# Kernel optimization log

Measured on AMD Instinct MI355X. Metric: run time of the kernel, lower is better.

## Reference

```python
import jax, jax.numpy as jnp
import numpy as np

B, S, D, H, DH = 4, 2048, 512, 8, 64  # batch, seq, input_dim, heads, per-head output_dim


def setup_inputs() -> dict:
    key = jax.random.key(0)
    ks = jax.random.split(key, 10)
    scale = 0.02
    inp = {
        "x": jax.random.normal(ks[0], (B, S, D), dtype=jnp.float32),
        "biological_mask": jnp.ones((B, S), dtype=bool),
        "Wq": jax.random.normal(ks[1], (D, H * DH), dtype=jnp.float32) * scale,
        "bq": jnp.zeros((H * DH,), dtype=jnp.float32),
        "Wk": jax.random.normal(ks[2], (D, H * DH), dtype=jnp.float32) * scale,
        "bk": jnp.zeros((H * DH,), dtype=jnp.float32),
        "Wv": jax.random.normal(ks[3], (D, H * DH), dtype=jnp.float32) * scale,
        "bv": jnp.zeros((H * DH,), dtype=jnp.float32),
        "Wo": jax.random.normal(ks[4], (H * DH, DH), dtype=jnp.float32) * scale,
        "bo": jnp.zeros((DH,), dtype=jnp.float32),
        "prior_weight": jnp.full((1,), 0.1, dtype=jnp.float32),
    }
    return inp


def reference(x, biological_mask, Wq, bq, Wk, bk, Wv, bv, Wo, bo, prior_weight):
    b, s, _ = x.shape
    inv_sqrt_dh = jnp.float32(1.0 / np.sqrt(DH))
    # projections -> [B,H,S,DH]
    q = (x @ Wq + bq).reshape(b, s, H, DH).transpose(0, 2, 1, 3)
    k = (x @ Wk + bk).reshape(b, s, H, DH).transpose(0, 2, 1, 3)
    v = (x @ Wv + bv).reshape(b, s, H, DH).transpose(0, 2, 1, 3)
    # scores [B,H,S,S]
    scores = jnp.einsum("bhqd,bhkd->bhqk", q, k) * inv_sqrt_dh
    # biological prior: identity matrix, broadcast over batch and heads
    prior = jnp.eye(s, dtype=scores.dtype)[None, None, :, :]
    scores = scores + prior_weight[0] * prior
    attn = jax.nn.softmax(scores, axis=-1)  # dropout is identity in eval mode
    attended = jnp.einsum("bhqk,bhkd->bhqd", attn, v)
    attended = attended.transpose(0, 2, 1, 3).reshape(b, s, H * DH)
    return attended @ Wo + bo
```

## Files before the change

kernel.cpp:

```cpp
#include <hip/hip_runtime.h>
#include <hip/hip_bf16.h>

#define B_ 4
#define S_ 2048
#define D_ 512
#define H_ 8
#define DH_ 64
#define HD_ 512
#define M_ 8192
#define QKVN 1536
#define QKN 1024
#define LOG2E 1.4426950408889634f

typedef __attribute__((ext_vector_type(8))) short bf16x8;
typedef __attribute__((ext_vector_type(4))) float f32x4;
typedef unsigned short u16;

__device__ inline u16 f2bf(float f) {
    __hip_bfloat16 h = __float2bfloat16(f);
    return *reinterpret_cast<u16*>(&h);
}

__device__ inline void async_cp16(const void* g, void* l) {
    __builtin_amdgcn_global_load_lds(
        (const __attribute__((address_space(1))) unsigned int*)g,
        (__attribute__((address_space(3))) unsigned int*)l, 16, 0, 0);
}

__global__ __launch_bounds__(256) void prep_all(
    const float* __restrict__ x, const float* __restrict__ Wq,
    const float* __restrict__ Wk, const float* __restrict__ Wv,
    const float* __restrict__ Wo, u16* __restrict__ xb,
    u16* __restrict__ WqkvT, u16* __restrict__ WoT)
{
    const int z = blockIdx.z;
    const int tid = threadIdx.x;

    if (z == 4) {
        const int id = blockIdx.y * 64 + blockIdx.x;
#pragma unroll
        for (int it = 0; it < 4; ++it) {
            int i = it * 131072 + id * 256 + tid;
            float4 a = *reinterpret_cast<const float4*>(&x[(size_t)i * 8]);
            float4 b = *reinterpret_cast<const float4*>(&x[(size_t)i * 8 + 4]);
            bf16x8 o;
            o[0] = f2bf(a.x); o[1] = f2bf(a.y); o[2] = f2bf(a.z); o[3] = f2bf(a.w);
            o[4] = f2bf(b.x); o[5] = f2bf(b.y); o[6] = f2bf(b.z); o[7] = f2bf(b.w);
            *reinterpret_cast<bf16x8*>(&xb[(size_t)i * 8]) = o;
        }
        return;
    }

    const float* src; u16* dst; int R, C;
    if (z < 3) { if (blockIdx.x >= 8) return;
                 src = (z == 0) ? Wq : (z == 1) ? Wk : Wv;
                 dst = WqkvT + (size_t)z * 512 * 512; R = 512; C = 512; }
    else       { if (blockIdx.x) return; src = Wo; dst = WoT; R = 512; C = 64; }

    __shared__ u16 T[64][65];
    const int c0 = blockIdx.x * 64, r0 = blockIdx.y * 64;
#pragma unroll
    for (int i = 0; i < 4; ++i) {
        int idx = i * 256 + tid;
        int r = idx >> 4, q4 = (idx & 15) << 2;
        float4 vv = *reinterpret_cast<const float4*>(&src[(size_t)(r0 + r) * C + c0 + q4]);
        T[r][q4 + 0] = f2bf(vv.x); T[r][q4 + 1] = f2bf(vv.y);
        T[r][q4 + 2] = f2bf(vv.z); T[r][q4 + 3] = f2bf(vv.w);
    }
    __syncthreads();
#pragma unroll
    for (int i = 0; i < 2; ++i) {
        int idx = i * 256 + tid;
        int cc = idx >> 3, jj = idx & 7;
        bf16x8 o;
#pragma unroll
        for (int e = 0; e < 8; ++e) o[e] = (short)T[jj * 8 + e][cc];
        *reinterpret_cast<bf16x8*>(&dst[(size_t)(c0 + cc) * R + r0 + jj * 8]) = o;
    }
}

__global__ __launch_bounds__(256) void gemm_qkv(
    const u16* __restrict__ A, const u16* __restrict__ BT,
    const float* __restrict__ bq, const float* __restrict__ bk,
    const float* __restrict__ bv, u16* __restrict__ qk,
    u16* __restrict__ v3, float qscale)
{
    __shared__ __align__(16) u16 As[128 * 64];
    __shared__ __align__(16) u16 Bs[128 * 64];
    const int tid = threadIdx.x, lane = tid & 63, w = tid >> 6;
    const int l15 = lane & 15, l4 = lane >> 4;

    const int bidf = blockIdx.x;
    const int xcd = bidf & 7, pos = bidf >> 3;
    const int swz = xcd * 96 + pos;
    const int by = swz / 12, bx = swz - by * 12;
    const int tm = by * 128, tn = bx * 128;
    const int wm = (w >> 1) * 64, wn = (w & 1) * 64;

    f32x4 acc[4][4] = {};

    for (int k0 = 0; k0 < 512; k0 += 64) {
#pragma unroll
        for (int i = 0; i < 4; ++i) {
            int call = w * 4 + i;
            int c = call * 64 + lane;
            int r = c >> 3, j = c & 7;
            async_cp16(A + (size_t)(tm + r) * 512 + k0 + ((j ^ (r & 7)) << 3),
                       &As[call * 512]);
            async_cp16(BT + (size_t)(tn + r) * 512 + k0 + ((j ^ (r & 7)) << 3),
                       &Bs[call * 512]);
        }
        __syncthreads();
#pragma unroll
        for (int ks = 0; ks < 2; ++ks) {
            bf16x8 af[4], bf[4];
#pragma unroll
            for (int mf = 0; mf < 4; ++mf) {
                int r = wm + mf * 16 + l15;
                int j = ks * 4 + l4;
                af[mf] = *reinterpret_cast<const bf16x8*>(&As[(r * 8 + (j ^ (r & 7))) * 8]);
            }
#pragma unroll
            for (int nf = 0; nf < 4; ++nf) {
                int r = wn + nf * 16 + l15;
                int j = ks * 4 + l4;
                bf[nf] = *reinterpret_cast<const bf16x8*>(&Bs[(r * 8 + (j ^ (r & 7))) * 8]);
            }
#pragma unroll
            for (int mf = 0; mf < 4; ++mf)
#pragma unroll
                for (int nf = 0; nf < 4; ++nf)
                    acc[mf][nf] = __builtin_amdgcn_mfma_f32_16x16x32_bf16(
                        af[mf], bf[nf], acc[mf][nf], 0, 0, 0);
        }
        __syncthreads();
    }
#pragma unroll
    for (int nf = 0; nf < 4; ++nf) {
        const int col = tn + wn + nf * 16 + l15;
        if (col < QKN) {
            const float bias_v = (col < 512) ? bq[col] : bk[col - 512];
            const float scl = (col < 512) ? qscale : 1.0f;
#pragma unroll
            for (int mf = 0; mf < 4; ++mf)
#pragma unroll
                for (int r = 0; r < 4; ++r) {
                    int row = tm + wm + mf * 16 + l4 * 4 + r;
                    qk[(size_t)row * QKN + col] = f2bf((acc[mf][nf][r] + bias_v) * scl);
                }
        } else {
            const int dcol = col - QKN;
            const float bias_v = bv[dcol];
            const int hh = dcol >> 6, d64 = dcol & 63;
            const int n = d64 >> 4, dd = d64 & 15;
#pragma unroll
            for (int mf = 0; mf < 4; ++mf) {
                int row0 = tm + wm + mf * 16 + l4 * 4;
                int b = row0 >> 11, s = row0 & 2047;
                int t = s >> 6, s6 = s & 63;
                int ks = s6 >> 5, l4i = (s6 >> 3) & 3, kvi = s6 & 7;
                ushort4 pk;
                pk.x = f2bf(acc[mf][nf][0] + bias_v);
                pk.y = f2bf(acc[mf][nf][1] + bias_v);
                pk.z = f2bf(acc[mf][nf][2] + bias_v);
                pk.w = f2bf(acc[mf][nf][3] + bias_v);
                size_t idx = (((((size_t)(b * 8 + hh) * 32 + t) * 4 + n) * 2 + ks) * 4
                              + l4i) * 128 + dd * 8 + kvi;
                *reinterpret_cast<ushort4*>(&v3[idx]) = pk;
            }
        }
    }
}

__global__ __launch_bounds__(256, 4) void flash_mfma(
    const u16* __restrict__ qk, const u16* __restrict__ v3,
    const float* __restrict__ pw_ptr, u16* __restrict__ att)
{
    __shared__ __align__(16) u16 Kb[2][4096];

    const int tid = threadIdx.x, lane = tid & 63, w = tid >> 6;
    const int l15 = lane & 15, l4 = lane >> 4;
    const int bid = blockIdx.x;
    const int x = bid & 7, g = bid >> 3;
    const int bh = x * 4 + (g >> 5), qt = g & 31;
    const int h = bh & 7, b = bh >> 3;
    const float pwl = pw_ptr[0] * LOG2E;

    const u16* qbase = qk + (size_t)b * S_ * QKN + h * 64;
    const u16* kbase = qbase + 512;
    const u16* vbase = v3 + (size_t)bh * 32 * 4 * 2 * 512 + l4 * 128 + l15 * 8;

    const int qrow0 = qt * 64 + w * 16;
    bf16x8 qb[2];
#pragma unroll
    for (int ks2 = 0; ks2 < 2; ++ks2)
        qb[ks2] = *reinterpret_cast<const bf16x8*>(
            &qbase[(size_t)(qrow0 + l15) * QKN + ks2 * 32 + l4 * 8]);

    const bf16x8 ones = {(short)0x3F80, (short)0x3F80, (short)0x3F80, (short)0x3F80,
                         (short)0x3F80, (short)0x3F80, (short)0x3F80, (short)0x3F80};

    f32x4 accv[4] = {};
    f32x4 accl = {};
    const int diag_t = qt;

#define STAGE(buf, jj) do {                                                        \
    _Pragma("unroll")                                                              \
    for (int i_ = 0; i_ < 2; ++i_) {                                               \
        int call_ = w * 2 + i_;                                                    \
        int c_ = call_ * 64 + lane;                                                \
        int rho_ = c_ >> 3, j_ = c_ & 7;                                           \
        int pi_ = (rho_ & 32) | ((rho_ & 12) << 1) | ((rho_ & 16) >> 2)            \
                | (rho_ & 3);                                                      \
        async_cp16(kbase + (size_t)((jj) + pi_) * QKN + ((j_ ^ (rho_ & 7)) << 3),  \
                   &Kb[buf][call_ * 512]);                                         \
    } } while (0)

    STAGE(0, 0);
    __syncthreads();
    int cur = 0;

    for (int t = 0; t < 32; ++t) {
        const int j0 = t << 6;
        const u16* vt = vbase + (size_t)t * 4096;

        bf16x8 vb01[2][2];
#pragma unroll
        for (int n = 0; n < 2; ++n)
#pragma unroll
            for (int ks = 0; ks < 2; ++ks)
                vb01[n][ks] = *reinterpret_cast<const bf16x8*>(
                    vt + (n * 2 + ks) * 512);

        if (t < 31) STAGE(cur ^ 1, j0 + 64);

        f32x4 s[4] = {};
        __builtin_amdgcn_s_setprio(1);
#pragma unroll
        for (int c = 0; c < 4; ++c)
#pragma unroll
            for (int ks2 = 0; ks2 < 2; ++ks2) {
                const int rr = c * 16 + l15;
                const int sl = ks2 * 4 + l4;
                bf16x8 ka = *reinterpret_cast<const bf16x8*>(
                    &Kb[cur][(rr * 8 + (sl ^ (rr & 7))) * 8]);
                s[c] = __builtin_amdgcn_mfma_f32_16x16x32_bf16(ka, qb[ks2], s[c], 0, 0, 0);
            }
        __builtin_amdgcn_s_setprio(0);

        bf16x8 vb23[2][2];
#pragma unroll
        for (int n = 0; n < 2; ++n)
#pragma unroll
            for (int ks = 0; ks < 2; ++ks)
                vb23[n][ks] = *reinterpret_cast<const bf16x8*>(
                    vt + ((n + 2) * 2 + ks) * 512);

        if (t == diag_t) {
#pragma unroll
            for (int c = 0; c < 4; ++c)
#pragma unroll
                for (int r = 0; r < 4; ++r) {
                    int kv = (c >> 1) * 32 + l4 * 8 + (c & 1) * 4 + r;
                    if (j0 + kv == qrow0 + l15) s[c][r] += pwl;
                }
        }

        bf16x8 pa[2];
#pragma unroll
        for (int ks = 0; ks < 2; ++ks)
#pragma unroll
            for (int d2 = 0; d2 < 2; ++d2)
#pragma unroll
                for (int r = 0; r < 4; ++r)
                    pa[ks][d2 * 4 + r] = (short)f2bf(exp2f(s[ks * 2 + d2][r]));

        __builtin_amdgcn_s_setprio(1);
        accl = __builtin_amdgcn_mfma_f32_16x16x32_bf16(pa[0], ones, accl, 0, 0, 0);
        accl = __builtin_amdgcn_mfma_f32_16x16x32_bf16(pa[1], ones, accl, 0, 0, 0);
#pragma unroll
        for (int n = 0; n < 2; ++n)
#pragma unroll
            for (int ks = 0; ks < 2; ++ks)
                accv[n] = __builtin_amdgcn_mfma_f32_16x16x32_bf16(
                    pa[ks], vb01[n][ks], accv[n], 0, 0, 0);
#pragma unroll
        for (int n = 0; n < 2; ++n)
#pragma unroll
            for (int ks = 0; ks < 2; ++ks)
                accv[n + 2] = __builtin_amdgcn_mfma_f32_16x16x32_bf16(
                    pa[ks], vb23[n][ks], accv[n + 2], 0, 0, 0);
        __builtin_amdgcn_s_setprio(0);

        __syncthreads();
        cur ^= 1;
    }
#undef STAGE

#pragma unroll
    for (int r = 0; r < 4; ++r) {
        float inv = 1.0f / accl[r];
        int row = qrow0 + l4 * 4 + r;
#pragma unroll
        for (int nf = 0; nf < 4; ++nf)
            att[(size_t)(b * S_ + row) * HD_ + h * 64 + nf * 16 + l15] =
                f2bf(accv[nf][r] * inv);
    }
}

__global__ __launch_bounds__(64) void out_proj(
    const u16* __restrict__ att, const u16* __restrict__ WoT,
    const float* __restrict__ bo, float* __restrict__ out)
{
    const int lane = threadIdx.x;
    const int l15 = lane & 15, l4 = lane >> 4;
    const int row0 = blockIdx.x * 16;

    f32x4 acc[4] = {};
#pragma unroll 4
    for (int ks = 0; ks < 16; ++ks) {
        bf16x8 a = *reinterpret_cast<const bf16x8*>(
            &att[(size_t)(row0 + l15) * 512 + ks * 32 + l4 * 8]);
#pragma unroll
        for (int nf = 0; nf < 4; ++nf) {
            bf16x8 bb = *reinterpret_cast<const bf16x8*>(
                &WoT[(size_t)(nf * 16 + l15) * 512 + ks * 32 + l4 * 8]);
            acc[nf] = __builtin_amdgcn_mfma_f32_16x16x32_bf16(a, bb, acc[nf], 0, 0, 0);
        }
    }
#pragma unroll
    for (int nf = 0; nf < 4; ++nf) {
        int n = nf * 16 + l15;
        float bias_v = bo[n];
#pragma unroll
        for (int r = 0; r < 4; ++r)
            out[(size_t)(row0 + l4 * 4 + r) * 64 + n] = acc[nf][r] + bias_v;
    }
}

extern "C" void kernel_launch(void* const* d_in, const int* in_sizes, int n_in,
                              void* d_out, int out_size, void* d_ws, size_t ws_size,
                              hipStream_t stream)
{
    const float* x  = (const float*)d_in[0];
    const float* Wq = (const float*)d_in[2];
    const float* bq = (const float*)d_in[3];
    const float* Wk = (const float*)d_in[4];
    const float* bk = (const float*)d_in[5];
    const float* Wv = (const float*)d_in[6];
    const float* bv = (const float*)d_in[7];
    const float* Wo = (const float*)d_in[8];
    const float* bo = (const float*)d_in[9];
    const float* pw = (const float*)d_in[10];

    u16* ws = (u16*)d_ws;
    size_t o = 0;
    u16* xb    = ws + o; o += (size_t)M_ * D_;
    u16* WqkvT = ws + o; o += (size_t)QKVN * D_;
    u16* WoT   = ws + o; o += (size_t)DH_ * HD_;
    u16* qkb   = ws + o; o += (size_t)M_ * QKN;
    u16* v3b   = ws + o; o += (size_t)M_ * HD_;
    u16* att   = ws + o; o += (size_t)M_ * HD_;

    dim3 blk(256);
    prep_all<<<dim3(64, 8, 5), blk, 0, stream>>>(x, Wq, Wk, Wv, Wo, xb, WqkvT, WoT);

    gemm_qkv<<<dim3(768), blk, 0, stream>>>(
        xb, WqkvT, bq, bk, bv, qkb, v3b, 0.125f * LOG2E);

    flash_mfma<<<dim3(1024), blk, 0, stream>>>(qkb, v3b, pw, att);

    out_proj<<<dim3(M_ / 16), dim3(64), 0, stream>>>(att, WoT, bo, (float*)d_out);
}
```

Measured before the change: 99.68 us.

## Stage 128-key K tiles per barrier in flash kernel and split-K out_proj

The flash attention kernel now stages 128 K rows per double-buffer slot and processes two 64-key halves between barriers. This halves the number of __syncthreads and async-copy rounds, at the cost of doubling K shared memory to 32 KB per block, which may limit occupancy. The output projection moves to 256-thread blocks covering 32 rows, with a two-way split over K whose partial sums are reduced through shared memory. This gives fewer, fuller blocks.

Result: no change. 98.87 us (median of 3 runs) (-0.8%).

```diff
diff --git a/kernel.cpp b/kernel.cpp
--- a/kernel.cpp
+++ b/kernel.cpp
@@ -176,7 +176,7 @@
     const u16* __restrict__ qk, const u16* __restrict__ v3,
     const float* __restrict__ pw_ptr, u16* __restrict__ att)
 {
-    __shared__ __align__(16) u16 Kb[2][4096];
+    __shared__ __align__(16) u16 Kb[2][8192];
 
     const int tid = threadIdx.x, lane = tid & 63, w = tid >> 6;
     const int l15 = lane & 15, l4 = lane >> 4;
@@ -202,100 +202,105 @@
 
     f32x4 accv[4] = {};
     f32x4 accl = {};
-    const int diag_t = qt;
-
-#define STAGE(buf, jj) do {                                                        \
+
+#define STAGE2(buf, jj) do {                                                       \
     _Pragma("unroll")                                                              \
-    for (int i_ = 0; i_ < 2; ++i_) {                                               \
-        int call_ = w * 2 + i_;                                                    \
+    for (int i_ = 0; i_ < 4; ++i_) {                                               \
+        int call_ = w * 4 + i_;                                                    \
         int c_ = call_ * 64 + lane;                                                \
         int rho_ = c_ >> 3, j_ = c_ & 7;                                           \
-        int pi_ = (rho_ & 32) | ((rho_ & 12) << 1) | ((rho_ & 16) >> 2)            \
-                | (rho_ & 3);                                                      \
-        async_cp16(kbase + (size_t)((jj) + pi_) * QKN + ((j_ ^ (rho_ & 7)) << 3),  \
+        int r6_ = rho_ & 63;                                                       \
+        int pi_ = (rho_ & 64) | (r6_ & 32) | ((r6_ & 12) << 1)                     \
+                | ((r6_ & 16) >> 2) | (r6_ & 3);                                   \
+        async_cp16(kbase + (size_t)((jj) + pi_) * QKN + ((j_ ^ (r6_ & 7)) << 3),   \
                    &Kb[buf][call_ * 512]);                                         \
     } } while (0)
 
-    STAGE(0, 0);
+    STAGE2(0, 0);
     __syncthreads();
     int cur = 0;
 
-    for (int t = 0; t < 32; ++t) {
-        const int j0 = t << 6;
-        const u16* vt = vbase + (size_t)t * 4096;
-
-        bf16x8 vb01[2][2];
-#pragma unroll
-        for (int n = 0; n < 2; ++n)
+    for (int t = 0; t < 16; ++t) {
+        if (t < 15) STAGE2(cur ^ 1, (t + 1) << 7);
+
+#pragma unroll
+        for (int half = 0; half < 2; ++half) {
+            const int t2 = t * 2 + half;
+            const int j0h = t2 << 6;
+            const u16* vt = vbase + (size_t)t2 * 4096;
+            const u16* kb = &Kb[cur][half * 4096];
+
+            bf16x8 vb01[2][2];
+#pragma unroll
+            for (int n = 0; n < 2; ++n)
+#pragma unroll
+                for (int ks = 0; ks < 2; ++ks)
+                    vb01[n][ks] = *reinterpret_cast<const bf16x8*>(
+                        vt + (n * 2 + ks) * 512);
+
+            f32x4 s[4] = {};
+            __builtin_amdgcn_s_setprio(1);
+#pragma unroll
+            for (int c = 0; c < 4; ++c)
+#pragma unroll
+                for (int ks2 = 0; ks2 < 2; ++ks2) {
+                    const int rr = c * 16 + l15;
+                    const int sl = ks2 * 4 + l4;
+                    bf16x8 ka = *reinterpret_cast<const bf16x8*>(
+                        &kb[(rr * 8 + (sl ^ (rr & 7))) * 8]);
+                    s[c] = __builtin_amdgcn_mfma_f32_16x16x32_bf16(ka, qb[ks2], s[c], 0, 0, 0);
+                }
+            __builtin_amdgcn_s_setprio(0);
+
+            bf16x8 vb23[2][2];
+#pragma unroll
+            for (int n = 0; n < 2; ++n)
+#pragma unroll
+                for (int ks = 0; ks < 2; ++ks)
+                    vb23[n][ks] = *reinterpret_cast<const bf16x8*>(
+                        vt + ((n + 2) * 2 + ks) * 512);
+
+            if (t2 == qt) {
+#pragma unroll
+                for (int c = 0; c < 4; ++c)
+#pragma unroll
+                    for (int r = 0; r < 4; ++r) {
+                        int kv = (c >> 1) * 32 + l4 * 8 + (c & 1) * 4 + r;
+                        if (j0h + kv == qrow0 + l15) s[c][r] += pwl;
+                    }
+            }
+
+            bf16x8 pa[2];
 #pragma unroll
             for (int ks = 0; ks < 2; ++ks)
-                vb01[n][ks] = *reinterpret_cast<const bf16x8*>(
-                    vt + (n * 2 + ks) * 512);
-
-        if (t < 31) STAGE(cur ^ 1, j0 + 64);
-
-        f32x4 s[4] = {};
-        __builtin_amdgcn_s_setprio(1);
-#pragma unroll
-        for (int c = 0; c < 4; ++c)
-#pragma unroll
-            for (int ks2 = 0; ks2 < 2; ++ks2) {
-                const int rr = c * 16 + l15;
-                const int sl = ks2 * 4 + l4;
-                bf16x8 ka = *reinterpret_cast<const bf16x8*>(
-                    &Kb[cur][(rr * 8 + (sl ^ (rr & 7))) * 8]);
-                s[c] = __builtin_amdgcn_mfma_f32_16x16x32_bf16(ka, qb[ks2], s[c], 0, 0, 0);
-            }
-        __builtin_amdgcn_s_setprio(0);
-
-        bf16x8 vb23[2][2];
-#pragma unroll
-        for (int n = 0; n < 2; ++n)
-#pragma unroll
-            for (int ks = 0; ks < 2; ++ks)
-                vb23[n][ks] = *reinterpret_cast<const bf16x8*>(
-                    vt + ((n + 2) * 2 + ks) * 512);
-
-        if (t == diag_t) {
-#pragma unroll
-            for (int c = 0; c < 4; ++c)
-#pragma unroll
-                for (int r = 0; r < 4; ++r) {
-                    int kv = (c >> 1) * 32 + l4 * 8 + (c & 1) * 4 + r;
-                    if (j0 + kv == qrow0 + l15) s[c][r] += pwl;
-                }
-        }
-
-        bf16x8 pa[2];
-#pragma unroll
-        for (int ks = 0; ks < 2; ++ks)
-#pragma unroll
-            for (int d2 = 0; d2 < 2; ++d2)
-#pragma unroll
-                for (int r = 0; r < 4; ++r)
-                    pa[ks][d2 * 4 + r] = (short)f2bf(exp2f(s[ks * 2 + d2][r]));
-
-        __builtin_amdgcn_s_setprio(1);
-        accl = __builtin_amdgcn_mfma_f32_16x16x32_bf16(pa[0], ones, accl, 0, 0, 0);
-        accl = __builtin_amdgcn_mfma_f32_16x16x32_bf16(pa[1], ones, accl, 0, 0, 0);
-#pragma unroll
-        for (int n = 0; n < 2; ++n)
-#pragma unroll
-            for (int ks = 0; ks < 2; ++ks)
-                accv[n] = __builtin_amdgcn_mfma_f32_16x16x32_bf16(
-                    pa[ks], vb01[n][ks], accv[n], 0, 0, 0);
-#pragma unroll
-        for (int n = 0; n < 2; ++n)
-#pragma unroll
-            for (int ks = 0; ks < 2; ++ks)
-                accv[n + 2] = __builtin_amdgcn_mfma_f32_16x16x32_bf16(
-                    pa[ks], vb23[n][ks], accv[n + 2], 0, 0, 0);
-        __builtin_amdgcn_s_setprio(0);
+#pragma unroll
+                for (int d2 = 0; d2 < 2; ++d2)
+#pragma unroll
+                    for (int r = 0; r < 4; ++r)
+                        pa[ks][d2 * 4 + r] = (short)f2bf(exp2f(s[ks * 2 + d2][r]));
+
+            __builtin_amdgcn_s_setprio(1);
+            accl = __builtin_amdgcn_mfma_f32_16x16x32_bf16(pa[0], ones, accl, 0, 0, 0);
+            accl = __builtin_amdgcn_mfma_f32_16x16x32_bf16(pa[1], ones, accl, 0, 0, 0);
+#pragma unroll
+            for (int n = 0; n < 2; ++n)
+#pragma unroll
+                for (int ks = 0; ks < 2; ++ks)
+                    accv[n] = __builtin_amdgcn_mfma_f32_16x16x32_bf16(
+                        pa[ks], vb01[n][ks], accv[n], 0, 0, 0);
+#pragma unroll
+            for (int n = 0; n < 2; ++n)
+#pragma unroll
+                for (int ks = 0; ks < 2; ++ks)
+                    accv[n + 2] = __builtin_amdgcn_mfma_f32_16x16x32_bf16(
+                        pa[ks], vb23[n][ks], accv[n + 2], 0, 0, 0);
+            __builtin_amdgcn_s_setprio(0);
+        }
 
         __syncthreads();
         cur ^= 1;
     }
-#undef STAGE
+#undef STAGE2
 
 #pragma unroll
     for (int r = 0; r < 4; ++r) {
@@ -308,33 +313,46 @@
     }
 }
 
-__global__ __launch_bounds__(64) void out_proj(
+__global__ __launch_bounds__(256) void out_proj(
     const u16* __restrict__ att, const u16* __restrict__ WoT,
     const float* __restrict__ bo, float* __restrict__ out)
 {
-    const int lane = threadIdx.x;
+    __shared__ float red[32][65];
+    const int tid = threadIdx.x, lane = tid & 63, w = tid >> 6;
     const int l15 = lane & 15, l4 = lane >> 4;
-    const int row0 = blockIdx.x * 16;
+    const int row0 = blockIdx.x * 32;
+    const int rsub = (w & 1) * 16, kh = w >> 1;
 
     f32x4 acc[4] = {};
-#pragma unroll 4
-    for (int ks = 0; ks < 16; ++ks) {
+#pragma unroll
+    for (int ks = 0; ks < 8; ++ks) {
         bf16x8 a = *reinterpret_cast<const bf16x8*>(
-            &att[(size_t)(row0 + l15) * 512 + ks * 32 + l4 * 8]);
+            &att[(size_t)(row0 + rsub + l15) * 512 + (kh * 8 + ks) * 32 + l4 * 8]);
 #pragma unroll
         for (int nf = 0; nf < 4; ++nf) {
             bf16x8 bb = *reinterpret_cast<const bf16x8*>(
-                &WoT[(size_t)(nf * 16 + l15) * 512 + ks * 32 + l4 * 8]);
+                &WoT[(size_t)(nf * 16 + l15) * 512 + (kh * 8 + ks) * 32 + l4 * 8]);
             acc[nf] = __builtin_amdgcn_mfma_f32_16x16x32_bf16(a, bb, acc[nf], 0, 0, 0);
         }
     }
-#pragma unroll
-    for (int nf = 0; nf < 4; ++nf) {
-        int n = nf * 16 + l15;
-        float bias_v = bo[n];
-#pragma unroll
-        for (int r = 0; r < 4; ++r)
-            out[(size_t)(row0 + l4 * 4 + r) * 64 + n] = acc[nf][r] + bias_v;
+    if (kh == 1) {
+#pragma unroll
+        for (int nf = 0; nf < 4; ++nf)
+#pragma unroll
+            for (int r = 0; r < 4; ++r)
+                red[rsub + l4 * 4 + r][nf * 16 + l15] = acc[nf][r];
+    }
+    __syncthreads();
+    if (kh == 0) {
+#pragma unroll
+        for (int nf = 0; nf < 4; ++nf) {
+            int n = nf * 16 + l15;
+            float bias_v = bo[n];
+#pragma unroll
+            for (int r = 0; r < 4; ++r)
+                out[(size_t)(row0 + rsub + l4 * 4 + r) * 64 + n] =
+                    acc[nf][r] + red[rsub + l4 * 4 + r][n] + bias_v;
+        }
     }
 }
 
@@ -370,5 +388,5 @@
 
     flash_mfma<<<dim3(1024), blk, 0, stream>>>(qkb, v3b, pw, att);
 
-    out_proj<<<dim3(M_ / 16), dim3(64), 0, stream>>>(att, WoT, bo, (float*)d_out);
-}
+    out_proj<<<dim3(256), blk, 0, stream>>>(att, WoT, bo, (float*)d_out);
+}
```

## Stage part of V tile via async LDS copy; split out_proj K across waves

Applied to the files above, without the earlier changes.

In the flash kernel, the first 16-column slice of each V tile is now loaded asynchronously into a double-buffered LDS area together with the K tile. The remaining slices are still read directly from global memory into registers. This is meant to reduce per-lane global V loads and hide their latency, at the cost of extra LDS. Separately, out_proj now runs 256-thread blocks that each cover 32 rows, splitting the K dimension across two wave pairs and summing the halves through shared memory, which gives more parallelism per block for an extra sync.

Result: no change. 101.2 us (+1.6%).

```diff
diff --git a/kernel.cpp b/kernel.cpp
--- a/kernel.cpp
+++ b/kernel.cpp
@@ -177,6 +177,7 @@
     const float* __restrict__ pw_ptr, u16* __restrict__ att)
 {
     __shared__ __align__(16) u16 Kb[2][4096];
+    __shared__ __align__(16) u16 Vh[2][1024];
 
     const int tid = threadIdx.x, lane = tid & 63, w = tid >> 6;
     const int l15 = lane & 15, l4 = lane >> 4;
@@ -188,7 +189,8 @@
 
     const u16* qbase = qk + (size_t)b * S_ * QKN + h * 64;
     const u16* kbase = qbase + 512;
-    const u16* vbase = v3 + (size_t)bh * 32 * 4 * 2 * 512 + l4 * 128 + l15 * 8;
+    const u16* vtile0 = v3 + (size_t)bh * 32 * 4 * 2 * 512;
+    const u16* vbase = vtile0 + lane * 8;
 
     const int qrow0 = qt * 64 + w * 16;
     bf16x8 qb[2];
@@ -204,7 +206,8 @@
     f32x4 accl = {};
     const int diag_t = qt;
 
-#define STAGE(buf, jj) do {                                                        \
+#define STAGE(buf, tt) do {                                                        \
+    const int jj_ = (tt) << 6;                                                     \
     _Pragma("unroll")                                                              \
     for (int i_ = 0; i_ < 2; ++i_) {                                               \
         int call_ = w * 2 + i_;                                                    \
@@ -212,9 +215,13 @@
         int rho_ = c_ >> 3, j_ = c_ & 7;                                           \
         int pi_ = (rho_ & 32) | ((rho_ & 12) << 1) | ((rho_ & 16) >> 2)            \
                 | (rho_ & 3);                                                      \
-        async_cp16(kbase + (size_t)((jj) + pi_) * QKN + ((j_ ^ (rho_ & 7)) << 3),  \
+        async_cp16(kbase + (size_t)(jj_ + pi_) * QKN + ((j_ ^ (rho_ & 7)) << 3),   \
                    &Kb[buf][call_ * 512]);                                         \
-    } } while (0)
+    }                                                                              \
+    if (w < 2)                                                                     \
+        async_cp16(vtile0 + (size_t)(tt) * 4096 + w * 512 + lane * 8,              \
+                   &Vh[buf][w * 512]);                                             \
+    } while (0)
 
     STAGE(0, 0);
     __syncthreads();
@@ -224,15 +231,21 @@
         const int j0 = t << 6;
         const u16* vt = vbase + (size_t)t * 4096;
 
-        bf16x8 vb01[2][2];
+        bf16x8 vb12[2][2];
 #pragma unroll
         for (int n = 0; n < 2; ++n)
 #pragma unroll
             for (int ks = 0; ks < 2; ++ks)
-                vb01[n][ks] = *reinterpret_cast<const bf16x8*>(
-                    vt + (n * 2 + ks) * 512);
-
-        if (t < 31) STAGE(cur ^ 1, j0 + 64);
+                vb12[n][ks] = *reinterpret_cast<const bf16x8*>(
+                    vt + ((n + 1) * 2 + ks) * 512);
+
+        if (t < 31) STAGE(cur ^ 1, t + 1);
+
+        bf16x8 vb0[2];
+#pragma unroll
+        for (int ks = 0; ks < 2; ++ks)
+            vb0[ks] = *reinterpret_cast<const bf16x8*>(
+                &Vh[cur][ks * 512 + lane * 8]);
 
         f32x4 s[4] = {};
         __builtin_amdgcn_s_setprio(1);
@@ -248,13 +261,11 @@
             }
         __builtin_amdgcn_s_setprio(0);
 
-        bf16x8 vb23[2][2];
-#pragma unroll
-        for (int n = 0; n < 2; ++n)
-#pragma unroll
-            for (int ks = 0; ks < 2; ++ks)
-                vb23[n][ks] = *reinterpret_cast<const bf16x8*>(
-                    vt + ((n + 2) * 2 + ks) * 512);
+        bf16x8 vb3[2];
+#pragma unroll
+        for (int ks = 0; ks < 2; ++ks)
+            vb3[ks] = *reinterpret_cast<const bf16x8*>(
+                vt + (3 * 2 + ks) * 512);
 
         if (t == diag_t) {
 #pragma unroll
@@ -279,17 +290,19 @@
         accl = __builtin_amdgcn_mfma_f32_16x16x32_bf16(pa[0], ones, accl, 0, 0, 0);
         accl = __builtin_amdgcn_mfma_f32_16x16x32_bf16(pa[1], ones, accl, 0, 0, 0);
 #pragma unroll
+        for (int ks = 0; ks < 2; ++ks)
+            accv[0] = __builtin_amdgcn_mfma_f32_16x16x32_bf16(
+                pa[ks], vb0[ks], accv[0], 0, 0, 0);
+#pragma unroll
         for (int n = 0; n < 2; ++n)
 #pragma unroll
             for (int ks = 0; ks < 2; ++ks)
-                accv[n] = __builtin_amdgcn_mfma_f32_16x16x32_bf16(
-                    pa[ks], vb01[n][ks], accv[n], 0, 0, 0);
-#pragma unroll
-        for (int n = 0; n < 2; ++n)
-#pragma unroll
-            for (int ks = 0; ks < 2; ++ks)
-                accv[n + 2] = __builtin_amdgcn_mfma_f32_16x16x32_bf16(
-                    pa[ks], vb23[n][ks], accv[n + 2], 0, 0, 0);
+                accv[n + 1] = __builtin_amdgcn_mfma_f32_16x16x32_bf16(
+                    pa[ks], vb12[n][ks], accv[n + 1], 0, 0, 0);
+#pragma unroll
+        for (int ks = 0; ks < 2; ++ks)
+            accv[3] = __builtin_amdgcn_mfma_f32_16x16x32_bf16(
+                pa[ks], vb3[ks], accv[3], 0, 0, 0);
         __builtin_amdgcn_s_setprio(0);
 
         __syncthreads();
@@ -308,33 +321,46 @@
     }
 }
 
-__global__ __launch_bounds__(64) void out_proj(
+__global__ __launch_bounds__(256) void out_proj(
     const u16* __restrict__ att, const u16* __restrict__ WoT,
     const float* __restrict__ bo, float* __restrict__ out)
 {
-    const int lane = threadIdx.x;
+    __shared__ float red[32][65];
+    const int tid = threadIdx.x, lane = tid & 63, w = tid >> 6;
     const int l15 = lane & 15, l4 = lane >> 4;
-    const int row0 = blockIdx.x * 16;
+    const int row0 = blockIdx.x * 32;
+    const int rsub = (w & 1) * 16, kh = w >> 1;
 
     f32x4 acc[4] = {};
-#pragma unroll 4
-    for (int ks = 0; ks < 16; ++ks) {
+#pragma unroll
+    for (int ks = 0; ks < 8; ++ks) {
         bf16x8 a = *reinterpret_cast<const bf16x8*>(
-            &att[(size_t)(row0 + l15) * 512 + ks * 32 + l4 * 8]);
+            &att[(size_t)(row0 + rsub + l15) * 512 + (kh * 8 + ks) * 32 + l4 * 8]);
 #pragma unroll
         for (int nf = 0; nf < 4; ++nf) {
             bf16x8 bb = *reinterpret_cast<const bf16x8*>(
-                &WoT[(size_t)(nf * 16 + l15) * 512 + ks * 32 + l4 * 8]);
+                &WoT[(size_t)(nf * 16 + l15) * 512 + (kh * 8 + ks) * 32 + l4 * 8]);
             acc[nf] = __builtin_amdgcn_mfma_f32_16x16x32_bf16(a, bb, acc[nf], 0, 0, 0);
         }
     }
-#pragma unroll
-    for (int nf = 0; nf < 4; ++nf) {
-        int n = nf * 16 + l15;
-        float bias_v = bo[n];
-#pragma unroll
-        for (int r = 0; r < 4; ++r)
-            out[(size_t)(row0 + l4 * 4 + r) * 64 + n] = acc[nf][r] + bias_v;
+    if (kh == 1) {
+#pragma unroll
+        for (int nf = 0; nf < 4; ++nf)
+#pragma unroll
+            for (int r = 0; r < 4; ++r)
+                red[rsub + l4 * 4 + r][nf * 16 + l15] = acc[nf][r];
+    }
+    __syncthreads();
+    if (kh == 0) {
+#pragma unroll
+        for (int nf = 0; nf < 4; ++nf) {
+            int n = nf * 16 + l15;
+            float bias_v = bo[n];
+#pragma unroll
+            for (int r = 0; r < 4; ++r)
+                out[(size_t)(row0 + rsub + l4 * 4 + r) * 64 + n] =
+                    acc[nf][r] + red[rsub + l4 * 4 + r][n] + bias_v;
+        }
     }
 }
 
@@ -370,5 +396,5 @@
 
     flash_mfma<<<dim3(1024), blk, 0, stream>>>(qkb, v3b, pw, att);
 
-    out_proj<<<dim3(M_ / 16), dim3(64), 0, stream>>>(att, WoT, bo, (float*)d_out);
-}
+    out_proj<<<dim3(256), blk, 0, stream>>>(att, WoT, bo, (float*)d_out);
+}
```
